# Kernel optimization log

Measured on AMD Instinct MI355X. Metric: run time of the kernel, lower is better.

## Reference

```python
import jax, jax.numpy as jnp
import numpy as np

N = 50000
E = 800000
IN_DIM = 256
HID = 64
HEADS = 4
OUT_DIM = 40
NEG_SLOPE = 0.2


def _gatv2_conv(x, src, dst, Wl, bl, Wr, br, att, bias, concat):
    """PyG GATv2Conv (share_weights=False, eval mode, no attn dropout).
    src -> message source nodes, dst -> target nodes (softmax over dst)."""
    H, C = att.shape
    n = x.shape[0]
    xl = (x @ Wl + bl).reshape(n, H, C)  # source/message transform (lin_l)
    xr = (x @ Wr + br).reshape(n, H, C)  # target transform (lin_r)
    # per-edge logits: [E, H]
    s = xl[src] + xr[dst]                                  # [E,H,C]
    e = jnp.einsum('ehc,hc->eh', jax.nn.leaky_relu(s, NEG_SLOPE), att)
    # segment softmax over incoming edges of each target node
    m = jax.ops.segment_max(e, dst, num_segments=n)        # [N,H]
    m = jnp.where(jnp.isfinite(m), m, 0.0)                 # empty segments
    ex = jnp.exp(e - m[dst])
    denom = jax.ops.segment_sum(ex, dst, num_segments=n)   # [N,H]
    alpha = ex / (denom[dst] + 1e-16)                      # [E,H]
    out = jax.ops.segment_sum(alpha[:, :, None] * xl[src], dst, num_segments=n)
    if concat:
        out = out.reshape(n, H * C)
    else:
        out = out.mean(axis=1)
    return out + bias


def setup_inputs() -> dict:
    key = jax.random.key(0)
    ks = jax.random.split(key, 12)
    sc = 0.05
    return {
        'x': jax.random.normal(ks[0], (N, IN_DIM), jnp.float32),
        'src': jax.random.randint(ks[1], (E,), 0, N, jnp.int32),
        'dst': jax.random.randint(ks[2], (E,), 0, N, jnp.int32),
        'Wl1': jax.random.normal(ks[3], (IN_DIM, HEADS * HID), jnp.float32) * sc,
        'bl1': jnp.zeros((HEADS * HID,), jnp.float32),
        'Wr1': jax.random.normal(ks[4], (IN_DIM, HEADS * HID), jnp.float32) * sc,
        'br1': jnp.zeros((HEADS * HID,), jnp.float32),
        'att1': jax.random.normal(ks[5], (HEADS, HID), jnp.float32) * sc,
        'bias1': jnp.zeros((HEADS * HID,), jnp.float32),
        'Wl2': jax.random.normal(ks[6], (HEADS * HID, HEADS * HID), jnp.float32) * sc,
        'bl2': jnp.zeros((HEADS * HID,), jnp.float32),
        'Wr2': jax.random.normal(ks[7], (HEADS * HID, HEADS * HID), jnp.float32) * sc,
        'br2': jnp.zeros((HEADS * HID,), jnp.float32),
        'att2': jax.random.normal(ks[8], (HEADS, HID), jnp.float32) * sc,
        'bias2': jnp.zeros((HID,), jnp.float32),
        'Wc': jax.random.normal(ks[9], (HID, OUT_DIM), jnp.float32) * sc,
        'bc': jnp.zeros((OUT_DIM,), jnp.float32),
    }


def reference(x, src, dst, Wl1, bl1, Wr1, br1, att1, bias1,
              Wl2, bl2, Wr2, br2, att2, bias2, Wc, bc):
    h = _gatv2_conv(x, src, dst, Wl1, bl1, Wr1, br1, att1, bias1, concat=True)
    h = jax.nn.relu(h)  # dropout p applied only in training; eval -> identity
    h = _gatv2_conv(h, src, dst, Wl2, bl2, Wr2, br2, att2, bias2, concat=False)
    h = jax.nn.relu(h)
    return h @ Wc + bc  # [N, OUT_DIM]
```

## Files before the change

kernel.cpp:

```cpp
#include <hip/hip_runtime.h>
#include <hip/hip_bf16.h>
#include <math.h>


#define IN_DIM 256
#define HIDHC 256
#define HID 64
#define OUT_DIM 40

using half8  = __attribute__((ext_vector_type(8))) _Float16;
using half4  = __attribute__((ext_vector_type(4))) _Float16;
using half2v = __attribute__((ext_vector_type(2))) _Float16;
using f32x4  = __attribute__((ext_vector_type(4))) float;

__device__ __forceinline__ void gload16(const void* g, void* l) {
    __builtin_amdgcn_global_load_lds(
        (const __attribute__((address_space(1))) void*)g,
        (__attribute__((address_space(3))) void*)l, 16, 0, 0);
}


__global__ void edge_hist(const int* __restrict__ dst, int* __restrict__ deg, int E) {
    int i = blockIdx.x * blockDim.x + threadIdx.x;
    if (i < E) atomicAdd(&deg[dst[i]], 1);
}

__global__ void deg_block_reduce(const int* __restrict__ deg, int* __restrict__ bsum, int n) {
    int i = blockIdx.x * 256 + threadIdx.x;
    int v = (i < n) ? deg[i] : 0;
    #pragma unroll
    for (int off = 32; off; off >>= 1) v += __shfl_xor(v, off, 64);
    __shared__ int ws[4];
    int lane = threadIdx.x & 63, wid = threadIdx.x >> 6;
    if (lane == 0) ws[wid] = v;
    __syncthreads();
    if (threadIdx.x == 0) bsum[blockIdx.x] = ws[0] + ws[1] + ws[2] + ws[3];
}

__global__ void scan_bsums(const int* __restrict__ bsum, int* __restrict__ bpre, int nb) {
    __shared__ int s[256];
    int tid = threadIdx.x;
    int orig = (tid < nb) ? bsum[tid] : 0;
    s[tid] = orig;
    __syncthreads();
    #pragma unroll
    for (int off = 1; off < 256; off <<= 1) {
        int t = (tid >= off) ? s[tid - off] : 0;
        __syncthreads();
        s[tid] += t;
        __syncthreads();
    }
    if (tid < nb) bpre[tid] = s[tid] - orig;
}

__global__ void deg_scan_apply(const int* __restrict__ deg, const int* __restrict__ bpre,
                               int* __restrict__ offsets, int* __restrict__ cursor, int n) {
    int i = blockIdx.x * 256 + threadIdx.x;
    int lane = threadIdx.x & 63, wid = threadIdx.x >> 6;
    int v = (i < n) ? deg[i] : 0;
    int inc = v;
    #pragma unroll
    for (int off = 1; off < 64; off <<= 1) {
        int t = __shfl_up(inc, off, 64);
        if (lane >= off) inc += t;
    }
    __shared__ int ws[4];
    if (lane == 63) ws[wid] = inc;
    __syncthreads();
    int add = bpre[blockIdx.x];
    for (int w = 0; w < wid; ++w) add += ws[w];
    int incl = inc + add;
    if (i < n) { offsets[i + 1] = incl; cursor[i] = incl - v; }
    if (i == 0) offsets[0] = 0;
}

__global__ void edge_scatter(const int* __restrict__ src, const int* __restrict__ dst,
                             int* __restrict__ cursor, int* __restrict__ csr_src, int E) {
    int i = blockIdx.x * blockDim.x + threadIdx.x;
    if (i < E) {
        int p = atomicAdd(&cursor[dst[i]], 1);
        csr_src[p] = src[i];
    }
}


__global__ void cvt_f16(const float* __restrict__ in, _Float16* __restrict__ out, int n4) {
    int i = blockIdx.x * blockDim.x + threadIdx.x;
    if (i >= n4) return;
    float4 v = ((const float4*)in)[i];
    half4 h = { (_Float16)v.x, (_Float16)v.y, (_Float16)v.z, (_Float16)v.w };
    ((half4*)out)[i] = h;
}

__global__ void prep_weights(const float* __restrict__ W0, const float* __restrict__ W1,
                             const float* __restrict__ W2, const float* __restrict__ W3,
                             _Float16* __restrict__ T) {
    const float* Wsel = (blockIdx.y == 0) ? W0 : (blockIdx.y == 1) ? W1
                      : (blockIdx.y == 2) ? W2 : W3;
    int k = blockIdx.x, nn = threadIdx.x;
    float v = Wsel[k * 256 + nn];
    T[(size_t)blockIdx.y * 65536 + (size_t)nn * 256 + k] = (_Float16)v;
}


__global__ __launch_bounds__(512, 2) void gemm_dual(
    const _Float16* __restrict__ A,
    const _Float16* __restrict__ W0, const float* __restrict__ b0, _Float16* __restrict__ C0,
    const _Float16* __restrict__ W1, const float* __restrict__ b1, _Float16* __restrict__ C1,
    int M)
{
    __shared__ __align__(16) _Float16 sA[2][4096];
    __shared__ __align__(16) _Float16 sW[2][2][8192];

    int tid = threadIdx.x;
    int bm = blockIdx.x * 128;

    int lane = tid & 63, w = tid >> 6;
    int z = w >> 2, wq = w & 3;
    int r = lane & 15, q = lane >> 4;
    int m0 = (wq >> 1) * 64, n0 = (wq & 1) * 64;

    int akg  = (tid >> 7) * 8;
    int arow = min(bm + (tid & 127), M - 1);
    int alds = tid * 8;

    int wzi[4], wro[4], wkg[4], wld[4];
    #pragma unroll
    for (int i = 0; i < 4; ++i) {
        int g2 = tid + 512 * i;
        wzi[i] = g2 >> 10;
        int rem = g2 & 1023;
        int kgroup = rem >> 8;
        int row = rem & 255;
        wro[i] = row;
        wkg[i] = kgroup * 8;
        wld[i] = (kgroup * 256 + row) * 8;
    }

    f32x4 acc[2][4][4];
    #pragma unroll
    for (int nt = 0; nt < 2; ++nt)
        #pragma unroll
        for (int i = 0; i < 4; ++i)
            #pragma unroll
            for (int j = 0; j < 4; ++j) acc[nt][i][j] = (f32x4)0.f;

    gload16(A + (size_t)arow * 256 + akg, &sA[0][alds]);
    #pragma unroll
    for (int i = 0; i < 4; ++i) {
        const _Float16* wp = wzi[i] ? W1 : W0;
        gload16(wp + (size_t)wro[i] * 256 + wkg[i], &sW[0][wzi[i]][wld[i]]);
    }
    __builtin_amdgcn_s_waitcnt(0);
    __syncthreads();

    #pragma unroll 1
    for (int kt = 0; kt < 8; ++kt) {
        int buf = kt & 1;
        if (kt < 7) {
            int k0 = (kt + 1) * 32;
            gload16(A + (size_t)arow * 256 + k0 + akg, &sA[buf ^ 1][alds]);
            #pragma unroll
            for (int i = 0; i < 4; ++i) {
                const _Float16* wp = wzi[i] ? W1 : W0;
                gload16(wp + (size_t)wro[i] * 256 + k0 + wkg[i], &sW[buf ^ 1][wzi[i]][wld[i]]);
            }
        }
        half8 a[4];
        #pragma unroll
        for (int i = 0; i < 4; ++i)
            a[i] = *(const half8*)(&sA[buf][(q * 128 + m0 + i * 16 + r) * 8]);
        #pragma unroll
        for (int nt = 0; nt < 2; ++nt) {
            half8 b[4];
            #pragma unroll
            for (int j = 0; j < 4; ++j)
                b[j] = *(const half8*)(&sW[buf][z][(q * 256 + nt * 128 + n0 + j * 16 + r) * 8]);
            #pragma unroll
            for (int i = 0; i < 4; ++i)
                #pragma unroll
                for (int j = 0; j < 4; ++j)
                    acc[nt][i][j] = __builtin_amdgcn_mfma_f32_16x16x32_f16(a[i], b[j], acc[nt][i][j], 0, 0, 0);
        }
        __builtin_amdgcn_s_waitcnt(0);
        __syncthreads();
    }

    const float* bias = z ? b1 : b0;
    _Float16*    C    = z ? C1 : C0;

    #pragma unroll
    for (int nt = 0; nt < 2; ++nt) {
        float bv[4];
        #pragma unroll
        for (int j = 0; j < 4; ++j) bv[j] = bias[nt * 128 + n0 + j * 16 + r];
        #pragma unroll
        for (int i = 0; i < 4; ++i) {
            #pragma unroll
            for (int reg = 0; reg < 4; ++reg) {
                int orow = bm + m0 + i * 16 + q * 4 + reg;
                if (orow < M) {
                    #pragma unroll
                    for (int j = 0; j < 4; ++j)
                        C[(size_t)orow * 256 + nt * 128 + n0 + j * 16 + r] =
                            (_Float16)(acc[nt][i][j][reg] + bv[j]);
                }
            }
        }
    }
}


__global__ __launch_bounds__(256) void gat_node(
    const _Float16* __restrict__ xl, const _Float16* __restrict__ xr,
    const float* __restrict__ att, const float* __restrict__ bias,
    const int* __restrict__ offsets, const int* __restrict__ csr_src,
    void* __restrict__ out0, int n, int mode)
{
    int wid = threadIdx.x >> 6;
    int node = (blockIdx.x << 2) + wid;
    if (node >= n) return;
    int lane = threadIdx.x & 63;
    int H = lane >> 5;
    int p = lane & 31;

    const half2v c02 = { (_Float16)0.2f, (_Float16)0.2f };

    half8 xrh = *(const half8*)(xr + (size_t)node * HIDHC + p * 8);
    half2v xr01 = __builtin_shufflevector(xrh, xrh, 0, 1);
    half2v xr23 = __builtin_shufflevector(xrh, xrh, 2, 3);
    half2v xr45 = __builtin_shufflevector(xrh, xrh, 4, 5);
    half2v xr67 = __builtin_shufflevector(xrh, xrh, 6, 7);

    float4 af0 = *(const float4*)(att + p * 8);
    float4 af1 = *(const float4*)(att + p * 8 + 4);
    half2v at01 = { (_Float16)af0.x, (_Float16)af0.y };
    half2v at23 = { (_Float16)af0.z, (_Float16)af0.w };
    half2v at45 = { (_Float16)af1.x, (_Float16)af1.y };
    half2v at67 = { (_Float16)af1.z, (_Float16)af1.w };

    float acc[8];
    #pragma unroll
    for (int k = 0; k < 8; ++k) acc[k] = 0.f;
    float d = 0.f;

    auto edge_compute = [&](half8 h) {
        half2v h01 = __builtin_shufflevector(h, h, 0, 1);
        half2v h23 = __builtin_shufflevector(h, h, 2, 3);
        half2v h45 = __builtin_shufflevector(h, h, 4, 5);
        half2v h67 = __builtin_shufflevector(h, h, 6, 7);
        half2v s01 = h01 + xr01, s23 = h23 + xr23, s45 = h45 + xr45, s67 = h67 + xr67;
        half2v l01 = __builtin_elementwise_max(s01, s01 * c02);
        half2v l23 = __builtin_elementwise_max(s23, s23 * c02);
        half2v l45 = __builtin_elementwise_max(s45, s45 * c02);
        half2v l67 = __builtin_elementwise_max(s67, s67 * c02);
        float e = __builtin_amdgcn_fdot2(l01, at01, 0.f, false);
        e = __builtin_amdgcn_fdot2(l23, at23, e, false);
        e = __builtin_amdgcn_fdot2(l45, at45, e, false);
        e = __builtin_amdgcn_fdot2(l67, at67, e, false);
        e += __shfl_xor(e, 1);
        e += __shfl_xor(e, 2);
        e += __shfl_xor(e, 4);
        float pw = __expf(e);
        d += pw;
        #pragma unroll
        for (int k = 0; k < 8; ++k) acc[k] = fmaf(pw, (float)h[k], acc[k]);
    };

    int j0 = __builtin_amdgcn_readfirstlane(offsets[node]);
    int j1 = __builtin_amdgcn_readfirstlane(offsets[node + 1]);
    int deg = j1 - j0;

    int fast = min(deg, 64);
    int npf = fast >> 1;
    int idxv = 0;
    if (lane < fast) idxv = csr_src[j0 + lane];

    half8 hA, hB;
    if (npf > 0) { int s = __shfl(idxv, 0 + H, 64); hA = *(const half8*)(xl + (size_t)s * HIDHC + p * 8); }
    if (npf > 1) { int s = __shfl(idxv, 2 + H, 64); hB = *(const half8*)(xl + (size_t)s * HIDHC + p * 8); }
    int t = 0;
    for (; t + 4 <= npf; t += 2) {
        half8 ha = hA, hb = hB;
        { int s = __shfl(idxv, (t + 2) * 2 + H, 64); hA = *(const half8*)(xl + (size_t)s * HIDHC + p * 8); }
        { int s = __shfl(idxv, (t + 3) * 2 + H, 64); hB = *(const half8*)(xl + (size_t)s * HIDHC + p * 8); }
        edge_compute(ha);
        edge_compute(hb);
    }
    if (t + 2 <= npf) {
        half8 ha = hA, hb = hB;
        if (t + 2 < npf) { int s = __shfl(idxv, (t + 2) * 2 + H, 64); hA = *(const half8*)(xl + (size_t)s * HIDHC + p * 8); }
        edge_compute(ha);
        edge_compute(hb);
        t += 2;
    }
    if (t < npf) {
        edge_compute(hA);
    }

    int j = j0 + (npf << 1);
    for (; j + 2 <= j1; j += 2) {
        int s0 = __builtin_amdgcn_readfirstlane(csr_src[j]);
        int s1 = __builtin_amdgcn_readfirstlane(csr_src[j + 1]);
        int s = H ? s1 : s0;
        half8 h = *(const half8*)(xl + (size_t)s * HIDHC + p * 8);
        edge_compute(h);
    }
    if (j < j1) {
        int s0 = __builtin_amdgcn_readfirstlane(csr_src[j]);
        half8 h = *(const half8*)(xl + (size_t)s0 * HIDHC + p * 8);
        half2v h01 = __builtin_shufflevector(h, h, 0, 1);
        half2v h23 = __builtin_shufflevector(h, h, 2, 3);
        half2v h45 = __builtin_shufflevector(h, h, 4, 5);
        half2v h67 = __builtin_shufflevector(h, h, 6, 7);
        half2v s01 = h01 + xr01, s23 = h23 + xr23, s45 = h45 + xr45, s67 = h67 + xr67;
        half2v l01 = __builtin_elementwise_max(s01, s01 * c02);
        half2v l23 = __builtin_elementwise_max(s23, s23 * c02);
        half2v l45 = __builtin_elementwise_max(s45, s45 * c02);
        half2v l67 = __builtin_elementwise_max(s67, s67 * c02);
        float e = __builtin_amdgcn_fdot2(l01, at01, 0.f, false);
        e = __builtin_amdgcn_fdot2(l23, at23, e, false);
        e = __builtin_amdgcn_fdot2(l45, at45, e, false);
        e = __builtin_amdgcn_fdot2(l67, at67, e, false);
        e += __shfl_xor(e, 1);
        e += __shfl_xor(e, 2);
        e += __shfl_xor(e, 4);
        float pw = (H == 0) ? __expf(e) : 0.f;
        d += pw;
        #pragma unroll
        for (int k = 0; k < 8; ++k) acc[k] = fmaf(pw, (float)h[k], acc[k]);
    }

    d += __shfl_xor(d, 32);
    #pragma unroll
    for (int k = 0; k < 8; ++k) acc[k] += __shfl_xor(acc[k], 32);

    float inv = 1.f / (d + 1e-16f);
    float o[8];
    #pragma unroll
    for (int k = 0; k < 8; ++k) o[k] = acc[k] * inv;

    if (mode == 0) {
        if (H == 0) {
            float4 b0 = *(const float4*)(bias + p * 8);
            float4 b1 = *(const float4*)(bias + p * 8 + 4);
            float bb[8] = { b0.x, b0.y, b0.z, b0.w, b1.x, b1.y, b1.z, b1.w };
            half8 hh;
            #pragma unroll
            for (int k = 0; k < 8; ++k) hh[k] = (_Float16)fmaxf(o[k] + bb[k], 0.f);
            *(half8*)((_Float16*)out0 + (size_t)node * HIDHC + p * 8) = hh;
        }
    } else {
        #pragma unroll
        for (int k = 0; k < 8; ++k) {
            o[k] += __shfl_xor(o[k], 8);
            o[k] += __shfl_xor(o[k], 16);
        }
        if (lane < 8) {
            float4 b0 = *(const float4*)(bias + p * 8);
            float4 b1 = *(const float4*)(bias + p * 8 + 4);
            float bb[8] = { b0.x, b0.y, b0.z, b0.w, b1.x, b1.y, b1.z, b1.w };
            float4 o0, o1;
            o0.x = fmaxf(o[0] * 0.25f + bb[0], 0.f);
            o0.y = fmaxf(o[1] * 0.25f + bb[1], 0.f);
            o0.z = fmaxf(o[2] * 0.25f + bb[2], 0.f);
            o0.w = fmaxf(o[3] * 0.25f + bb[3], 0.f);
            o1.x = fmaxf(o[4] * 0.25f + bb[4], 0.f);
            o1.y = fmaxf(o[5] * 0.25f + bb[5], 0.f);
            o1.z = fmaxf(o[6] * 0.25f + bb[6], 0.f);
            o1.w = fmaxf(o[7] * 0.25f + bb[7], 0.f);
            float* dst = (float*)out0 + (size_t)node * HID + p * 8;
            *(float4*)dst = o0;
            *(float4*)(dst + 4) = o1;
        }
    }
}


__global__ __launch_bounds__(256) void final_linear(
    const float* __restrict__ h2, const float* __restrict__ Wc,
    const float* __restrict__ bc, float* __restrict__ out, int n)
{
    __shared__ float Ws[HID * OUT_DIM];
    __shared__ float bs[OUT_DIM];
    __shared__ float hs[64][HID + 1];

    for (int i = threadIdx.x; i < HID * OUT_DIM; i += 256) Ws[i] = Wc[i];
    if (threadIdx.x < OUT_DIM) bs[threadIdx.x] = bc[threadIdx.x];

    int n0 = blockIdx.x * 64;
    for (int i = threadIdx.x; i < 64 * HID; i += 256) {
        int r = i >> 6, c = i & 63;
        int node = n0 + r;
        hs[r][c] = (node < n) ? h2[(size_t)node * HID + c] : 0.f;
    }
    __syncthreads();

    for (int idx = threadIdx.x; idx < 64 * OUT_DIM; idx += 256) {
        int r = idx / OUT_DIM, o = idx % OUT_DIM;
        int node = n0 + r;
        if (node < n) {
            float s = bs[o];
            #pragma unroll
            for (int c = 0; c < HID; ++c) s = fmaf(hs[r][c], Ws[c * OUT_DIM + o], s);
            out[(size_t)node * OUT_DIM + o] = s;
        }
    }
}


extern "C" void kernel_launch(void* const* d_in, const int* in_sizes, int n_in,
                              void* d_out, int out_size, void* d_ws, size_t ws_size,
                              hipStream_t stream) {
    const int N = in_sizes[0] / IN_DIM;
    const int E = in_sizes[1];

    const float* x    = (const float*)d_in[0];
    const int*   src  = (const int*)d_in[1];
    const int*   dst  = (const int*)d_in[2];
    const float* Wl1  = (const float*)d_in[3];
    const float* bl1  = (const float*)d_in[4];
    const float* Wr1  = (const float*)d_in[5];
    const float* br1  = (const float*)d_in[6];
    const float* att1 = (const float*)d_in[7];
    const float* bias1= (const float*)d_in[8];
    const float* Wl2  = (const float*)d_in[9];
    const float* bl2  = (const float*)d_in[10];
    const float* Wr2  = (const float*)d_in[11];
    const float* br2  = (const float*)d_in[12];
    const float* att2 = (const float*)d_in[13];
    const float* bias2= (const float*)d_in[14];
    const float* Wc   = (const float*)d_in[15];
    const float* bc   = (const float*)d_in[16];

    char* ws = (char*)d_ws;
    size_t off = 0;
    _Float16* xlh = (_Float16*)(ws + off); off += (size_t)N * HIDHC * 2;
    _Float16* xrh = (_Float16*)(ws + off); off += (size_t)N * HIDHC * 2;
    _Float16* Af  = (_Float16*)(ws + off); off += (size_t)N * HIDHC * 2;
    float*    h2  = (float*)(ws + off);    off += (size_t)N * HID * 4;
    _Float16* Wt  = (_Float16*)(ws + off); off += (size_t)4 * 65536 * 2;
    int* deg     = (int*)(ws + off); off += (size_t)N * 4;
    int* offsets = (int*)(ws + off); off += (size_t)(N + 1) * 4;
    int* cursor  = (int*)(ws + off); off += (size_t)N * 4;
    int* csr     = (int*)(ws + off); off += (size_t)E * 4;
    int* bsum    = (int*)(ws + off); off += 256 * 4;
    int* bpre    = (int*)(ws + off); off += 256 * 4;

    const int NB = (N + 255) / 256;

    hipMemsetAsync(deg, 0, (size_t)N * 4, stream);
    edge_hist<<<(E + 255) / 256, 256, 0, stream>>>(dst, deg, E);
    deg_block_reduce<<<NB, 256, 0, stream>>>(deg, bsum, N);
    scan_bsums<<<1, 256, 0, stream>>>(bsum, bpre, NB);
    deg_scan_apply<<<NB, 256, 0, stream>>>(deg, bpre, offsets, cursor, N);
    edge_scatter<<<(E + 255) / 256, 256, 0, stream>>>(src, dst, cursor, csr, E);
    prep_weights<<<dim3(256, 4), 256, 0, stream>>>(Wl1, Wr1, Wl2, Wr2, Wt);
    cvt_f16<<<(N * HIDHC / 4 + 255) / 256, 256, 0, stream>>>(x, Af, N * HIDHC / 4);

    const int KW = 65536;
    const int GB = (N + 127) / 128;
    gemm_dual<<<GB, 512, 0, stream>>>(Af,
        Wt + 0 * KW, bl1, xlh,
        Wt + 1 * KW, br1, xrh, N);
    gat_node<<<(N + 3) / 4, 256, 0, stream>>>(xlh, xrh, att1, bias1, offsets, csr,
                                              (void*)Af, N, 0);
    gemm_dual<<<GB, 512, 0, stream>>>(Af,
        Wt + 2 * KW, bl2, xlh,
        Wt + 3 * KW, br2, xrh, N);
    gat_node<<<(N + 3) / 4, 256, 0, stream>>>(xlh, xrh, att2, bias2, offsets, csr,
                                              (void*)h2, N, 1);
    final_linear<<<(N + 63) / 64, 256, 0, stream>>>(h2, Wc, bc, (float*)d_out, N);
}
```

Measured before the change: 451.4 us.

## Pre-tile GEMM operands into contiguous blocks and split N across grid

The A matrix (converted input and the layer-1 output) and the transposed weights are now written in a tile-packed layout, so each 32-wide k-slice of a 128-row tile is contiguous and one 16-byte global-to-LDS load per thread fills it. The GEMM grid gains a second dimension that splits the 256 output columns into two 128-wide halves, which halves per-block accumulators and LDS. The goal is simpler, fully coalesced loads with less address arithmetic, and more blocks for occupancy. The cost is that each A tile is now read twice, the scatter-style writes in the conversion and gat_node kernels become less contiguous, and an extra memset is added for the padded last tile.

```diff
diff --git a/kernel.cpp b/kernel.cpp
--- a/kernel.cpp
+++ b/kernel.cpp
@@ -84,12 +84,16 @@
 }
 
 
-__global__ void cvt_f16(const float* __restrict__ in, _Float16* __restrict__ out, int n4) {
+__global__ void cvt_f16_tiled(const float* __restrict__ in, _Float16* __restrict__ out, int n4) {
     int i = blockIdx.x * blockDim.x + threadIdx.x;
     if (i >= n4) return;
     float4 v = ((const float4*)in)[i];
     half4 h = { (_Float16)v.x, (_Float16)v.y, (_Float16)v.z, (_Float16)v.w };
-    ((half4*)out)[i] = h;
+    int node = i >> 6;
+    int kb = (i & 63) * 4;
+    size_t a = (size_t)(node >> 7) * 32768 + (size_t)(kb >> 3) * 1024
+             + (size_t)(node & 127) * 8 + (kb & 7);
+    *(half4*)(out + a) = h;
 }
 
 __global__ void prep_weights(const float* __restrict__ W0, const float* __restrict__ W1,
@@ -99,58 +103,45 @@
                       : (blockIdx.y == 2) ? W2 : W3;
     int k = blockIdx.x, nn = threadIdx.x;
     float v = Wsel[k * 256 + nn];
-    T[(size_t)blockIdx.y * 65536 + (size_t)nn * 256 + k] = (_Float16)v;
-}
-
-
-__global__ __launch_bounds__(512, 2) void gemm_dual(
-    const _Float16* __restrict__ A,
+    size_t a = (size_t)blockIdx.y * 65536
+             + (size_t)(nn >> 7) * 32768 + (size_t)(k >> 5) * 4096
+             + (size_t)((k >> 3) & 3) * 1024 + (size_t)(nn & 127) * 8 + (k & 7);
+    T[a] = (_Float16)v;
+}
+
+
+__global__ __launch_bounds__(512) void gemm_dual(
+    const _Float16* __restrict__ Apk,
     const _Float16* __restrict__ W0, const float* __restrict__ b0, _Float16* __restrict__ C0,
     const _Float16* __restrict__ W1, const float* __restrict__ b1, _Float16* __restrict__ C1,
     int M)
 {
     __shared__ __align__(16) _Float16 sA[2][4096];
-    __shared__ __align__(16) _Float16 sW[2][2][8192];
+    __shared__ __align__(16) _Float16 sW[2][2][4096];
 
     int tid = threadIdx.x;
     int bm = blockIdx.x * 128;
+    int bn = blockIdx.y * 128;
 
     int lane = tid & 63, w = tid >> 6;
-    int z = w >> 2, wq = w & 3;
+    int z  = w >> 2, wq = w & 3;
     int r = lane & 15, q = lane >> 4;
     int m0 = (wq >> 1) * 64, n0 = (wq & 1) * 64;
 
-    int akg  = (tid >> 7) * 8;
-    int arow = min(bm + (tid & 127), M - 1);
-    int alds = tid * 8;
-
-    int wzi[4], wro[4], wkg[4], wld[4];
-    #pragma unroll
-    for (int i = 0; i < 4; ++i) {
-        int g2 = tid + 512 * i;
-        wzi[i] = g2 >> 10;
-        int rem = g2 & 1023;
-        int kgroup = rem >> 8;
-        int row = rem & 255;
-        wro[i] = row;
-        wkg[i] = kgroup * 8;
-        wld[i] = (kgroup * 256 + row) * 8;
-    }
-
-    f32x4 acc[2][4][4];
-    #pragma unroll
-    for (int nt = 0; nt < 2; ++nt)
-        #pragma unroll
-        for (int i = 0; i < 4; ++i)
-            #pragma unroll
-            for (int j = 0; j < 4; ++j) acc[nt][i][j] = (f32x4)0.f;
-
-    gload16(A + (size_t)arow * 256 + akg, &sA[0][alds]);
-    #pragma unroll
-    for (int i = 0; i < 4; ++i) {
-        const _Float16* wp = wzi[i] ? W1 : W0;
-        gload16(wp + (size_t)wro[i] * 256 + wkg[i], &sW[0][wzi[i]][wld[i]]);
-    }
+    const _Float16* Abase = Apk + (size_t)blockIdx.x * 32768;
+    const _Float16* W0b   = W0  + (size_t)blockIdx.y * 32768;
+    const _Float16* W1b   = W1  + (size_t)blockIdx.y * 32768;
+    int go = tid * 8;
+
+    f32x4 acc[4][4];
+    #pragma unroll
+    for (int i = 0; i < 4; ++i)
+        #pragma unroll
+        for (int j = 0; j < 4; ++j) acc[i][j] = (f32x4)0.f;
+
+    gload16(Abase + go, &sA[0][go]);
+    gload16(W0b + go, &sW[0][0][go]);
+    gload16(W1b + go, &sW[0][1][go]);
     __builtin_amdgcn_s_waitcnt(0);
     __syncthreads();
 
@@ -158,53 +149,42 @@
     for (int kt = 0; kt < 8; ++kt) {
         int buf = kt & 1;
         if (kt < 7) {
-            int k0 = (kt + 1) * 32;
-            gload16(A + (size_t)arow * 256 + k0 + akg, &sA[buf ^ 1][alds]);
-            #pragma unroll
-            for (int i = 0; i < 4; ++i) {
-                const _Float16* wp = wzi[i] ? W1 : W0;
-                gload16(wp + (size_t)wro[i] * 256 + k0 + wkg[i], &sW[buf ^ 1][wzi[i]][wld[i]]);
-            }
-        }
-        half8 a[4];
+            int k0 = (kt + 1) * 4096;
+            gload16(Abase + k0 + go, &sA[buf ^ 1][go]);
+            gload16(W0b + k0 + go, &sW[buf ^ 1][0][go]);
+            gload16(W1b + k0 + go, &sW[buf ^ 1][1][go]);
+        }
+        half8 a[4], b[4];
+        #pragma unroll
+        for (int i = 0; i < 4; ++i) {
+            a[i] = *(const half8*)(&sA[buf][(q * 128 + m0 + i * 16 + r) * 8]);
+            b[i] = *(const half8*)(&sW[buf][z][(q * 128 + n0 + i * 16 + r) * 8]);
+        }
         #pragma unroll
         for (int i = 0; i < 4; ++i)
-            a[i] = *(const half8*)(&sA[buf][(q * 128 + m0 + i * 16 + r) * 8]);
-        #pragma unroll
-        for (int nt = 0; nt < 2; ++nt) {
-            half8 b[4];
             #pragma unroll
             for (int j = 0; j < 4; ++j)
-                b[j] = *(const half8*)(&sW[buf][z][(q * 256 + nt * 128 + n0 + j * 16 + r) * 8]);
-            #pragma unroll
-            for (int i = 0; i < 4; ++i)
+                acc[i][j] = __builtin_amdgcn_mfma_f32_16x16x32_f16(a[i], b[j], acc[i][j], 0, 0, 0);
+        __builtin_amdgcn_s_waitcnt(0);
+        __syncthreads();
+    }
+
+    const float* bias = z ? b1 : b0;
+    _Float16*    C    = z ? C1 : C0;
+
+    float bv[4];
+    #pragma unroll
+    for (int j = 0; j < 4; ++j) bv[j] = bias[bn + n0 + j * 16 + r];
+    #pragma unroll
+    for (int i = 0; i < 4; ++i) {
+        #pragma unroll
+        for (int reg = 0; reg < 4; ++reg) {
+            int orow = bm + m0 + i * 16 + q * 4 + reg;
+            if (orow < M) {
                 #pragma unroll
                 for (int j = 0; j < 4; ++j)
-                    acc[nt][i][j] = __builtin_amdgcn_mfma_f32_16x16x32_f16(a[i], b[j], acc[nt][i][j], 0, 0, 0);
-        }
-        __builtin_amdgcn_s_waitcnt(0);
-        __syncthreads();
-    }
-
-    const float* bias = z ? b1 : b0;
-    _Float16*    C    = z ? C1 : C0;
-
-    #pragma unroll
-    for (int nt = 0; nt < 2; ++nt) {
-        float bv[4];
-        #pragma unroll
-        for (int j = 0; j < 4; ++j) bv[j] = bias[nt * 128 + n0 + j * 16 + r];
-        #pragma unroll
-        for (int i = 0; i < 4; ++i) {
-            #pragma unroll
-            for (int reg = 0; reg < 4; ++reg) {
-                int orow = bm + m0 + i * 16 + q * 4 + reg;
-                if (orow < M) {
-                    #pragma unroll
-                    for (int j = 0; j < 4; ++j)
-                        C[(size_t)orow * 256 + nt * 128 + n0 + j * 16 + r] =
-                            (_Float16)(acc[nt][i][j][reg] + bv[j]);
-                }
+                    C[(size_t)orow * 256 + bn + n0 + j * 16 + r] =
+                        (_Float16)(acc[i][j][reg] + bv[j]);
             }
         }
     }
@@ -348,7 +328,9 @@
             half8 hh;
             #pragma unroll
             for (int k = 0; k < 8; ++k) hh[k] = (_Float16)fmaxf(o[k] + bb[k], 0.f);
-            *(half8*)((_Float16*)out0 + (size_t)node * HIDHC + p * 8) = hh;
+            _Float16* dst = (_Float16*)out0 + (size_t)(node >> 7) * 32768
+                          + (size_t)p * 1024 + (size_t)(node & 127) * 8;
+            *(half8*)dst = hh;
         }
     } else {
         #pragma unroll
@@ -435,9 +417,10 @@
 
     char* ws = (char*)d_ws;
     size_t off = 0;
+    const int NT = (N + 127) / 128;
     _Float16* xlh = (_Float16*)(ws + off); off += (size_t)N * HIDHC * 2;
     _Float16* xrh = (_Float16*)(ws + off); off += (size_t)N * HIDHC * 2;
-    _Float16* Af  = (_Float16*)(ws + off); off += (size_t)N * HIDHC * 2;
+    _Float16* Af  = (_Float16*)(ws + off); off += (size_t)NT * 32768 * 2;
     float*    h2  = (float*)(ws + off);    off += (size_t)N * HID * 4;
     _Float16* Wt  = (_Float16*)(ws + off); off += (size_t)4 * 65536 * 2;
     int* deg     = (int*)(ws + off); off += (size_t)N * 4;
@@ -450,22 +433,24 @@
     const int NB = (N + 255) / 256;
 
     hipMemsetAsync(deg, 0, (size_t)N * 4, stream);
+    if (N & 127)
+        hipMemsetAsync(Af + (size_t)(NT - 1) * 32768, 0, 32768 * 2, stream);
     edge_hist<<<(E + 255) / 256, 256, 0, stream>>>(dst, deg, E);
     deg_block_reduce<<<NB, 256, 0, stream>>>(deg, bsum, N);
     scan_bsums<<<1, 256, 0, stream>>>(bsum, bpre, NB);
     deg_scan_apply<<<NB, 256, 0, stream>>>(deg, bpre, offsets, cursor, N);
     edge_scatter<<<(E + 255) / 256, 256, 0, stream>>>(src, dst, cursor, csr, E);
     prep_weights<<<dim3(256, 4), 256, 0, stream>>>(Wl1, Wr1, Wl2, Wr2, Wt);
-    cvt_f16<<<(N * HIDHC / 4 + 255) / 256, 256, 0, stream>>>(x, Af, N * HIDHC / 4);
+    cvt_f16_tiled<<<(N * HIDHC / 4 + 255) / 256, 256, 0, stream>>>(x, Af, N * HIDHC / 4);
 
     const int KW = 65536;
-    const int GB = (N + 127) / 128;
-    gemm_dual<<<GB, 512, 0, stream>>>(Af,
+    dim3 gg(NT, 2);
+    gemm_dual<<<gg, 512, 0, stream>>>(Af,
         Wt + 0 * KW, bl1, xlh,
         Wt + 1 * KW, br1, xrh, N);
     gat_node<<<(N + 3) / 4, 256, 0, stream>>>(xlh, xrh, att1, bias1, offsets, csr,
                                               (void*)Af, N, 0);
-    gemm_dual<<<GB, 512, 0, stream>>>(Af,
+    gemm_dual<<<gg, 512, 0, stream>>>(Af,
         Wt + 2 * KW, bl2, xlh,
         Wt + 3 * KW, br2, xrh, N);
     gat_node<<<(N + 3) / 4, 256, 0, stream>>>(xlh, xrh, att2, bias2, offsets, csr,
```

After: 428.0 us. 1.05x faster.
